# Performance work log

Hardware: AMD Instinct MI355X
Metric: run time of the kernel (lower is better)

The kernel has to match this reference:

```python
import jax, jax.numpy as jnp
import numpy as np

NH, NB, E, R, K, SU = 64, 384, 1024, 1024, 16, 64  # humans, boxes, enc size, repr size, cardinality, sub-repr
C, P, SPA = 256, 7, 36
NUM_ITER = 2


def _ln(x, g, b):
    m = jnp.mean(x, -1, keepdims=True)
    v = jnp.mean((x - m) ** 2, -1, keepdims=True)
    return (x - m) / jnp.sqrt(v + 1e-5) * g + b


def setup_inputs():
    key = jax.random.key(0)
    it = iter(jax.random.split(key, 48))
    def w(shape, scale=0.02):
        return jax.random.normal(next(it), shape, dtype=jnp.float32) * scale
    z = lambda *s: jnp.zeros(s, jnp.float32)
    return {
        "box_feats": jax.random.normal(next(it), (NB, C, P, P), dtype=jnp.float32),
        "spatial_raw": jax.random.uniform(next(it), (NH * NB, SPA), dtype=jnp.float32),
        "features3": jax.random.normal(next(it), (1, C, P, P), dtype=jnp.float32),
        "Wb1": w((C * P * P, E)), "bb1": z(E), "Wb2": w((E, E)), "bb2": z(E),
        "Ws1": w((SPA, 128)), "bs1": z(128), "Ws2": w((128, 256)), "bs2": z(256),
        "Ws3": w((256, 1024)), "bs3": z(1024),
        "Wadj": w((R, 1)), "badj": z(1),
        "gh": jnp.ones((E,), jnp.float32), "bh": z(E),
        "go": jnp.ones((E,), jnp.float32), "bo": z(E),
        "A1": w((K, 2 * E, SU)), "Ab1": z(K, SU), "A2": w((K, 1024, SU)), "Ab2": z(K, SU),
        "A3": w((K, SU, R)), "Ab3": z(K, R),
        "G1": w((K, 256, SU)), "Gb1": z(K, SU), "G2": w((K, 1024, SU)), "Gb2": z(K, SU),
        "G3": w((K, SU, R)), "Gb3": z(K, R),
        "S1": w((K, E, SU)), "Sb1": z(K, SU), "S2": w((K, 1024, SU)), "Sb2": z(K, SU),
        "S3": w((K, SU, R)), "Sb3": z(K, R),
        "O1": w((K, E, SU)), "Ob1": z(K, SU), "O2": w((K, 1024, SU)), "Ob2": z(K, SU),
        "O3": w((K, SU, R)), "Ob3": z(K, R),
        "n_h": NH,
    }


def _forward(box_feats, spatial_raw, features3, Wb1, bb1, Wb2, bb2, Ws1, bs1, Ws2, bs2, Ws3, bs3,
             Wadj, badj, gh, bh, go, bo, A1, Ab1, A2, Ab2, A3, Ab3, G1, Gb1, G2, Gb2, G3, Gb3,
             S1, Sb1, S2, Sb2, S3, Sb3, O1, Ob1, O2, Ob2, O3, Ob3, n_h):
    n = box_feats.shape[0]
    # box_head: Flatten -> Linear -> ReLU -> Linear -> ReLU
    enc = jax.nn.relu(jax.nn.relu(box_feats.reshape(n, -1) @ Wb1 + bb1) @ Wb2 + bb2)  # [n, E]
    h, o = enc[:n_h], enc
    # spatial_head MLP on flat pairs (pair p = i*n + j, human i, object j)
    sp = spatial_raw
    for W, b in ((Ws1, bs1), (Ws2, bs2), (Ws3, bs3)):
        sp = jax.nn.relu(sp @ W + b)                      # [n_h*n, 1024]
    spr = sp.reshape(n_h, n, -1)
    gfeat = features3.mean((2, 3))                        # AdaptiveAvgPool2d(1) -> [1, 256]

    def mbf(app, W1, b1, W2, b2, W3, b3):
        # MultiBranchFusion over flat pairs, K branches vectorized as batched GEMMs
        a = jnp.einsum('pa,kau->kpu', app, W1) + b1[:, None, :]
        s = jnp.einsum('ps,ksu->kpu', sp, W2) + b2[:, None, :]
        m = jax.nn.relu(a * s)                            # [K, P, sub]
        return jax.nn.relu(jnp.einsum('kpu,kur->pr', m, W3) + b3.sum(0))

    def pair_app(hh, oo):
        return jnp.concatenate([jnp.repeat(hh, n, axis=0), jnp.tile(oo, (n_h, 1))], axis=1)

    adj = jnp.ones((n_h, n), sp.dtype)
    for _ in range(NUM_ITER):
        wts = mbf(pair_app(h, o), A1, Ab1, A2, Ab2, A3, Ab3)      # [P, R]
        adj = (wts @ Wadj + badj).reshape(n_h, n)
        # MessageMBF object->subject (_forward_object_nodes): output [n_h, n, R], no final relu
        ao = jnp.einsum('na,kau->knu', o, O1) + Ob1[:, None, :]
        so = jnp.einsum('hns,ksu->khnu', spr, O2) + Ob2[:, None, None, :]
        m_o2s = jnp.einsum('khnu,kur->hnr', jax.nn.relu(ao[:, None] * so), O3) + Ob3.sum(0)
        h = _ln(h + jax.nn.relu(jnp.sum(jax.nn.softmax(adj, 1)[..., None] * m_o2s, axis=1)), gh, bh)
        # MessageMBF subject->object (_forward_human_nodes): output [n, n_h, R]
        ah = jnp.einsum('ha,kau->khu', h, S1) + Sb1[:, None, :]
        sh = jnp.einsum('hns,ksu->khnu', spr, S2) + Sb2[:, None, None, :]
        m_s2o = jnp.einsum('khnu,kur->nhr', jax.nn.relu(ah[:, :, None, :] * sh), S3) + Sb3.sum(0)
        o = _ln(o + jax.nn.relu(jnp.sum(jax.nn.softmax(adj.T, 1)[..., None] * m_s2o, axis=1)), go, bo)

    attn = mbf(pair_app(h, o), A1, Ab1, A2, Ab2, A3, Ab3)          # [P, R]
    gp = jnp.broadcast_to(gfeat, (sp.shape[0], gfeat.shape[1]))
    attn_g = mbf(gp, G1, Gb1, G2, Gb2, G3, Gb3)                    # [P, R]
    return jnp.concatenate([attn, attn_g], axis=1)                 # [P, 2R]


def reference(box_feats, spatial_raw, features3, Wb1, bb1, Wb2, bb2, Ws1, bs1, Ws2, bs2, Ws3, bs3,
              Wadj, badj, gh, bh, go, bo, A1, Ab1, A2, Ab2, A3, Ab3, G1, Gb1, G2, Gb2, G3, Gb3,
              S1, Sb1, S2, Sb2, S3, Sb3, O1, Ob1, O2, Ob2, O3, Ob3, n_h):
    return _forward(box_feats, spatial_raw, features3, Wb1, bb1, Wb2, bb2, Ws1, bs1, Ws2, bs2, Ws3, bs3,
                    Wadj, badj, gh, bh, go, bo, A1, Ab1, A2, Ab2, A3, Ab3, G1, Gb1, G2, Gb2, G3, Gb3,
                    S1, Sb1, S2, Sb2, S3, Sb3, O1, Ob1, O2, Ob2, O3, Ob3, n_h)
```

## Files before the change

### kernel.cpp

```cpp
#include <hip/hip_runtime.h>
#include <hip/hip_bf16.h>
#include <cstdint>
#include <cstddef>

#define NH    64
#define NB    384
#define EDIM  1024
#define PAIRS (NH*NB)
#define SPA   36

using in_t  = float;
using out_t = float;
using sb_t  = __hip_bfloat16;

typedef short bf16x8 __attribute__((ext_vector_type(8)));
typedef float f32x4  __attribute__((ext_vector_type(4)));

static __device__ __forceinline__ float cvt(float x){ return x; }
static __device__ __forceinline__ float cvt(__hip_bfloat16 x){ return __bfloat162float(x); }
static __device__ __forceinline__ void stv(float* p, float v){ *p = v; }
static __device__ __forceinline__ void stv(__hip_bfloat16* p, float v){ *p = __float2bfloat16(v); }

static __device__ __forceinline__ float b2f(unsigned short u){
  union { unsigned int i; float f; } x; x.i = ((unsigned int)u)<<16; return x.f;
}

typedef const __attribute__((address_space(1))) void* as1_t;
typedef __attribute__((address_space(3))) void* as3_t;
static __device__ __forceinline__ void gl_lds16(const void* g, void* l){
  __builtin_amdgcn_global_load_lds((as1_t)g, (as3_t)l, 16, 0, 0);
}

#define POOL_BB1   0
#define POOL_BB2   1024
#define POOL_BS1   2048
#define POOL_BS2   2176
#define POOL_BS3   2432
#define POOL_AB1   3456
#define POOL_GB1   4480
#define POOL_SB1   5504
#define POOL_OB1   6528
#define POOL_B2ALL 7552
#define POOL_AB3S  11648
#define POOL_GB3S  12672
#define POOL_SB3S  13696
#define POOL_OB3S  14720
#define POOL_GFEAT 15744
#define POOL_TOTAL 16000

template<int EPI, int RELU, typename TC>
__global__ __launch_bounds__(256)
void gemm_mfma(int M, int N, int KS, int lda, int ldb,
               const sb_t* __restrict__ A,
               const sb_t* __restrict__ Bt,
               const float* __restrict__ bias,
               TC* __restrict__ C, int ldc, int coff, long long strideCz,
               const float* __restrict__ Wadj,
               const float* __restrict__ ab3s,
               float* __restrict__ adjOut)
{
  __shared__ alignas(16) short lA[2][128*32];
  __shared__ alignas(16) short lB[2][128*32];
  const int tid = threadIdx.x;
  const int w = tid >> 6, l = tid & 63;
  const int m0 = blockIdx.x * 128, n0 = blockIdx.y * 128;
  const int wr = w >> 1, wc = w & 1;
  const int Koff = blockIdx.z * KS;

  const int srow = w*32 + (l>>2);
  const int scol = (l&3)*8;
  const sb_t* gA = A  + (size_t)(m0 + srow)*(size_t)lda + Koff + scol;
  const sb_t* gB = Bt + (size_t)(n0 + srow)*(size_t)ldb + Koff + scol;
  short* lA0 = &lA[0][(w*32)*32];
  short* lA1 = &lA[1][(w*32)*32];
  short* lB0 = &lB[0][(w*32)*32];
  short* lB1 = &lB[1][(w*32)*32];

  f32x4 acc[4][4];
  const f32x4 zz = {0.f,0.f,0.f,0.f};
  #pragma unroll
  for (int i=0;i<4;++i)
    #pragma unroll
    for (int j=0;j<4;++j) acc[i][j] = zz;

  const int fr  = l & 15;
  const int fko = (l >> 4) * 8;

  for (int k0 = 0; k0 < KS; k0 += 64) {
    gl_lds16(gA + k0,               lA0);
    gl_lds16(gA + k0 + 16*lda,      lA0 + 16*32);
    gl_lds16(gA + k0 + 32,          lA1);
    gl_lds16(gA + k0 + 32 + 16*lda, lA1 + 16*32);
    gl_lds16(gB + k0,               lB0);
    gl_lds16(gB + k0 + 16*ldb,      lB0 + 16*32);
    gl_lds16(gB + k0 + 32,          lB1);
    gl_lds16(gB + k0 + 32 + 16*ldb, lB1 + 16*32);
    __syncthreads();
    #pragma unroll
    for (int kh=0; kh<2; ++kh) {
      bf16x8 af[4], bfv[4];
      #pragma unroll
      for (int i=0;i<4;++i)
        af[i]  = *(const bf16x8*)&lA[kh][(wr*64 + i*16 + fr)*32 + fko];
      #pragma unroll
      for (int j=0;j<4;++j)
        bfv[j] = *(const bf16x8*)&lB[kh][(wc*64 + j*16 + fr)*32 + fko];
      #pragma unroll
      for (int i=0;i<4;++i)
        #pragma unroll
        for (int j=0;j<4;++j)
          acc[i][j] = __builtin_amdgcn_mfma_f32_16x16x32_bf16(af[i], bfv[j], acc[i][j], 0, 0, 0);
    }
    __syncthreads();
  }

  const int cn = l & 15;
  const int cr = (l >> 4) * 4;

  if (EPI == 1) {
    float part[4][4];
    #pragma unroll
    for (int i=0;i<4;++i)
      #pragma unroll
      for (int r=0;r<4;++r) part[i][r] = 0.f;
    #pragma unroll
    for (int j=0;j<4;++j) {
      const int col = n0 + wc*64 + j*16 + cn;
      const float wv = Wadj[col];
      const float bv = ab3s[col];
      #pragma unroll
      for (int i=0;i<4;++i)
        #pragma unroll
        for (int r=0;r<4;++r)
          part[i][r] += fmaxf(acc[i][j][r] + bv, 0.f) * wv;
    }
    #pragma unroll
    for (int m=1;m<16;m<<=1)
      #pragma unroll
      for (int i=0;i<4;++i)
        #pragma unroll
        for (int r=0;r<4;++r)
          part[i][r] += __shfl_xor(part[i][r], m, 64);
    if (cn == 0) {
      #pragma unroll
      for (int i=0;i<4;++i)
        #pragma unroll
        for (int r=0;r<4;++r)
          atomicAdd(&adjOut[m0 + wr*64 + i*16 + cr + r], part[i][r]);
    }
    return;
  }

  #pragma unroll
  for (int j=0;j<4;++j) {
    const int col = n0 + wc*64 + j*16 + cn;
    const float bv = (EPI==0 && bias) ? bias[col] : 0.f;
    #pragma unroll
    for (int i=0;i<4;++i) {
      #pragma unroll
      for (int r=0;r<4;++r) {
        const int row = m0 + wr*64 + i*16 + cr + r;
        float v = acc[i][j][r] + bv;
        if (RELU) v = fmaxf(v, 0.f);
        if (EPI == 2)
          stv(&C[(size_t)blockIdx.z*strideCz + (size_t)row*ldc + col], v);
        else
          stv(&C[(size_t)row*ldc + coff + col], v);
      }
    }
  }
}

template<int EPI, int RELU, typename TC>
__global__ __launch_bounds__(512, 2)
void gemm256(int M, int N, int K, int lda, int ldb,
             const sb_t* __restrict__ A,
             const sb_t* __restrict__ Bt,
             const float* __restrict__ bias,
             TC* __restrict__ C, int ldc, int coff,
             const float* __restrict__ Wadj,
             const float* __restrict__ ab3s,
             float* __restrict__ adjOut)
{
  __shared__ alignas(16) short sh[2][2][256*64];

  const int tid = threadIdx.x;
  const int w = tid >> 6, l = tid & 63;
  const int wr = w >> 2, wc = w & 3;

  const unsigned gx = gridDim.x, gy = gridDim.y;
  const unsigned nwg = gx * gy;
  const unsigned hwid = blockIdx.x + gx * blockIdx.y;
  const unsigned q = nwg >> 3, rr = nwg & 7;
  const unsigned xcd = hwid & 7, jj = hwid >> 3;
  const unsigned wg = (xcd < rr ? xcd*(q+1) : rr*(q+1) + (xcd-rr)*q) + jj;
  const int by = (int)(wg % gy), bx = (int)(wg / gy);
  const int m0 = bx * 256, n0 = by * 256;

  const int NT = K >> 6;

  const int lr = l >> 3;
  const int lch = ((l & 7) ^ lr) * 8;

  auto stage = [&](int p, int s, int t){
    short* lbA = &sh[p][0][0];
    short* lbB = &sh[p][1][0];
    const int k0 = t * 64;
    #pragma unroll
    for (int c=0;c<2;++c){
      const int g = (w<<1) + c;
      int row0; const sb_t* mat; int ld; int rb; short* dst;
      if (s==0){ row0 = g*8;                              mat=Bt; ld=ldb; rb=n0; dst=lbB; }
      else if (s==1){ row0 = 128 + g*8;                   mat=Bt; ld=ldb; rb=n0; dst=lbB; }
      else if (s==2){ row0 = (g<8)? g*8    : 128+(g-8)*8; mat=A;  ld=lda; rb=m0; dst=lbA; }
      else          { row0 = (g<8)? 64+g*8 : 192+(g-8)*8; mat=A;  ld=lda; rb=m0; dst=lbA; }
      gl_lds16(mat + (size_t)(rb + row0 + lr)*(size_t)ld + k0 + lch, dst + row0*64);
    }
  };

  const int fr = l & 15;
  const int fg = l >> 4;
  const int sx = fr & 7;
  const int x0 = ((0 + fg) ^ sx) * 8;
  const int x1 = ((4 + fg) ^ sx) * 8;
  const int oA = (wr*128 + fr) * 64;
  const int oB = (wc*64  + fr) * 64;

  f32x4 acc[8][4];
  const f32x4 zz = {0.f,0.f,0.f,0.f};
  #pragma unroll
  for (int i=0;i<8;++i)
    #pragma unroll
    for (int j=0;j<4;++j) acc[i][j] = zz;

#define G256_BAR()   __builtin_amdgcn_s_barrier()
#define G256_LGKM0() asm volatile("s_waitcnt lgkmcnt(0)" ::: "memory")
#define G256_LGKM8() asm volatile("s_waitcnt lgkmcnt(8)" ::: "memory")
#define G256_VM(n)   asm volatile("s_waitcnt vmcnt(" #n ")" ::: "memory")
#define G256_LOADA(ph)                                                   \
  af[0][0] = *(const bf16x8*)(sa + oA + (2*(ph)+0)*1024 + x0);           \
  af[0][1] = *(const bf16x8*)(sa + oA + (2*(ph)+0)*1024 + x1);           \
  af[1][0] = *(const bf16x8*)(sa + oA + (2*(ph)+1)*1024 + x0);           \
  af[1][1] = *(const bf16x8*)(sa + oA + (2*(ph)+1)*1024 + x1)
#define G256_MFMA(ph)                                                    \
  do { __builtin_amdgcn_s_setprio(1);                                    \
    _Pragma("unroll") for (int ii=0; ii<2; ++ii)                         \
    _Pragma("unroll") for (int j=0; j<4; ++j)                            \
    _Pragma("unroll") for (int kk=0; kk<2; ++kk)                         \
      acc[2*(ph)+ii][j] = __builtin_amdgcn_mfma_f32_16x16x32_bf16(       \
          af[ii][kk], bf[j][kk], acc[2*(ph)+ii][j], 0, 0, 0);            \
    __builtin_amdgcn_s_setprio(0); } while(0)

  stage(0,0,0); stage(0,1,0); stage(0,2,0); stage(0,3,0);
  G256_VM(4);
  if (NT > 1) {
    stage(1,0,1); stage(1,1,1); stage(1,2,1);
    G256_VM(6);
  } else {
    G256_VM(0);
  }
  G256_BAR();

  for (int t=0; t<NT; ++t) {
    const int cur = t & 1, pn = cur ^ 1;
    short* sa  = &sh[cur][0][0];
    short* sb2 = &sh[cur][1][0];
    bf16x8 bf[4][2], af[2][2];

    #pragma unroll
    for (int j=0;j<4;++j){
      bf[j][0] = *(const bf16x8*)(sb2 + oB + j*1024 + x0);
      bf[j][1] = *(const bf16x8*)(sb2 + oB + j*1024 + x1);
    }
    G256_LOADA(0);
    if (t+1 < NT) stage(pn, 3, t+1);
    G256_LGKM8();
    G256_BAR(); G256_LGKM0();
    G256_MFMA(0);
    G256_BAR();

    G256_LOADA(1);
    if (t+2 < NT) stage(cur, 0, t+2);
    G256_BAR(); G256_LGKM0();
    G256_MFMA(1);
    G256_BAR();

    G256_LOADA(2);
    if (t+2 < NT) stage(cur, 1, t+2);
    G256_BAR(); G256_LGKM0();
    G256_MFMA(2);
    G256_BAR();

    G256_LOADA(3);
    if (t+2 < NT) stage(cur, 2, t+2);
    G256_BAR(); G256_LGKM0();
    G256_MFMA(3);
    if (t+1 < NT) {
      if (t+2 < NT) { G256_VM(6); } else { G256_VM(0); }
      G256_BAR();
    }
  }

#undef G256_BAR
#undef G256_LGKM0
#undef G256_LGKM8
#undef G256_VM
#undef G256_LOADA
#undef G256_MFMA

  const int cn = l & 15;
  const int cr = (l >> 4) * 4;

  if (EPI == 1) {
    float part[8][4];
    #pragma unroll
    for (int i=0;i<8;++i)
      #pragma unroll
      for (int r=0;r<4;++r) part[i][r] = 0.f;
    #pragma unroll
    for (int j=0;j<4;++j) {
      const int col = n0 + wc*64 + j*16 + cn;
      const float wv = Wadj[col];
      const float bv = ab3s[col];
      #pragma unroll
      for (int i=0;i<8;++i)
        #pragma unroll
        for (int r=0;r<4;++r)
          part[i][r] += fmaxf(acc[i][j][r] + bv, 0.f) * wv;
    }
    #pragma unroll
    for (int m=1;m<16;m<<=1)
      #pragma unroll
      for (int i=0;i<8;++i)
        #pragma unroll
        for (int r=0;r<4;++r)
          part[i][r] += __shfl_xor(part[i][r], m, 64);
    if (cn == 0) {
      #pragma unroll
      for (int i=0;i<8;++i)
        #pragma unroll
        for (int r=0;r<4;++r)
          atomicAdd(&adjOut[m0 + wr*128 + i*16 + cr + r], part[i][r]);
    }
    return;
  }

  #pragma unroll
  for (int j=0;j<4;++j) {
    const int col = n0 + wc*64 + j*16 + cn;
    const float bv = bias ? bias[col] : 0.f;
    #pragma unroll
    for (int i=0;i<8;++i) {
      #pragma unroll
      for (int r=0;r<4;++r) {
        const int row = m0 + wr*128 + i*16 + cr + r;
        float v = acc[i][j][r] + bv;
        if (RELU) v = fmaxf(v, 0.f);
        stv(&C[(size_t)row*ldc + coff + col], v);
      }
    }
  }
}

template<typename TC>
__global__ __launch_bounds__(256)
void gemm_valu(int M, int N, int K,
               const in_t* __restrict__ S, int ldsS,
               const in_t* __restrict__ B, int ldb, long long strideB,
               const float* __restrict__ bias,
               TC* __restrict__ C, int ldc, int reluOut)
{
  __shared__ float As[16][65];
  __shared__ float Bs[16][68];
  const int z  = blockIdx.z;
  const in_t* Bz = B + (long long)z * strideB;
  const int m0 = blockIdx.x * 64;
  const int n0 = blockIdx.y * 64;
  const int tid = threadIdx.x;
  const int tx = tid & 15;
  const int ty = tid >> 4;

  float acc[4][4];
  #pragma unroll
  for (int i=0;i<4;++i)
    #pragma unroll
    for (int j=0;j<4;++j) acc[i][j]=0.f;

  const int kTiles = (K + 15) >> 4;
  for (int kt=0; kt<kTiles; ++kt) {
    const int k0 = kt << 4;
    #pragma unroll
    for (int q=0;q<4;++q) {
      const int p = m0 + ty + 16*q;
      const int c = k0 + tx;
      As[tx][ty+16*q] = (p < M && c < K) ? S[(size_t)p*ldsS + c] : 0.f;
    }
    {
      const int n = tid & 63;
      #pragma unroll
      for (int q=0;q<4;++q) {
        const int kk = (tid >> 6) + 4*q;
        const int gk = k0 + kk;
        const int gn = n0 + n;
        Bs[kk][n] = (gk < K && gn < N) ? Bz[(size_t)gk*ldb + gn] : 0.f;
      }
    }
    __syncthreads();
    #pragma unroll
    for (int kk=0; kk<16; ++kk) {
      float a[4], b[4];
      #pragma unroll
      for (int i=0;i<4;++i) a[i] = As[kk][ty + 16*i];
      #pragma unroll
      for (int j=0;j<4;++j) b[j] = Bs[kk][tx + 16*j];
      #pragma unroll
      for (int i=0;i<4;++i)
        #pragma unroll
        for (int j=0;j<4;++j) acc[i][j] += a[i]*b[j];
    }
    __syncthreads();
  }
  #pragma unroll
  for (int i=0;i<4;++i) {
    const int r = m0 + ty + 16*i;
    if (r >= M) continue;
    #pragma unroll
    for (int j=0;j<4;++j) {
      const int nn = n0 + tx + 16*j;
      if (nn >= N) continue;
      const int ccol = z*N + nn;
      float v = acc[i][j];
      if (bias) v += bias[ccol];
      if (reluOut) v = fmaxf(v, 0.f);
      stv(&C[(size_t)r*ldc + ccol], v);
    }
  }
}

struct Prep17 { const in_t* p[17]; };

__global__ __launch_bounds__(256)
void prep_kernel(Prep17 a, float* __restrict__ pool)
{
  const int len[17] = {1024,1024,128,256,1024,1024,1024,1024,1024,1024,1024,1024,1024,
                       1024,1024,1024,1024};
  const int off[17] = {POOL_BB1,POOL_BB2,POOL_BS1,POOL_BS2,POOL_BS3,POOL_AB1,
                       POOL_B2ALL+0,
                       POOL_GB1,
                       POOL_B2ALL+3072,
                       POOL_SB1,
                       POOL_B2ALL+2048,
                       POOL_OB1,
                       POOL_B2ALL+1024,
                       POOL_AB3S,POOL_GB3S,POOL_SB3S,POOL_OB3S};
  const int j = blockIdx.x;
  const in_t* src = a.p[j];
  const int L = len[j], o = off[j];
  for (int i = threadIdx.x; i < L; i += blockDim.x) {
    if (j < 13) {
      pool[o+i] = src[i];
    } else {
      float s = 0.f;
      for (int k=0;k<16;++k) s += src[k*1024 + i];
      pool[o+i] = s;
    }
  }
}

__global__ __launch_bounds__(64)
void gfeat_kernel(const in_t* __restrict__ f3, float* __restrict__ g)
{
  const int c = blockIdx.x;
  const int t = threadIdx.x;
  float s = (t < 49) ? f3[c*49 + t] : 0.f;
  #pragma unroll
  for (int o=32;o>0;o>>=1) s += __shfl_down(s, o, 64);
  if (t == 0) g[c] = s * (1.0f/49.0f);
}

__global__ __launch_bounds__(256)
void tcvt_kernel(const float* __restrict__ in, sb_t* __restrict__ outT, int R, int C)
{
  __shared__ float t[64][65];
  const int r0 = blockIdx.x*64, c0 = blockIdx.y*64;
  const int x = threadIdx.x & 63, y = threadIdx.x >> 6;
  #pragma unroll 4
  for (int q=0;q<16;++q){ const int rl = q*4 + y; t[rl][x] = in[(size_t)(r0+rl)*C + c0 + x]; }
  __syncthreads();
  #pragma unroll 4
  for (int q=0;q<16;++q){ const int cl = q*4 + y; stv(&outT[(size_t)(c0+cl)*R + r0 + x], t[x][cl]); }
}

__global__ __launch_bounds__(256)
void pack_kt_kernel(const float* __restrict__ W, sb_t* __restrict__ PT, int Cdim)
{
  __shared__ float t[64][65];
  const int c0 = blockIdx.x*64; const int k = blockIdx.y;
  const int x = threadIdx.x & 63, y = threadIdx.x >> 6;
  #pragma unroll 4
  for (int q=0;q<16;++q){ const int cl = q*4 + y; t[cl][x] = W[((size_t)k*Cdim + c0 + cl)*64 + x]; }
  __syncthreads();
  #pragma unroll 4
  for (int q=0;q<16;++q){ const int u = q*4 + y; stv(&PT[((size_t)k*64 + u)*Cdim + c0 + x], t[x][u]); }
}

__global__ void cvt_kernel(const float* __restrict__ in, sb_t* __restrict__ o, int n){
  const int i = blockIdx.x*256 + threadIdx.x;
  if (i < n) stv(&o[i], in[i]);
}

__global__ __launch_bounds__(256)
void combine4_kernel(const float* __restrict__ part, const float* __restrict__ bias,
                     sb_t* __restrict__ o)
{
  const int i = blockIdx.x*256 + threadIdx.x;
  const int c = i & 1023;
  float v = part[i] + part[i+393216] + part[i+2*393216] + part[i+3*393216] + bias[c];
  stv(&o[i], fmaxf(v, 0.f));
}

__global__ __launch_bounds__(256)
void encpost_kernel(const float* __restrict__ oB, sb_t* __restrict__ oBb,
                    float* __restrict__ hB, sb_t* __restrict__ hBb)
{
  const int p = blockIdx.x; const int c = blockIdx.y*256 + threadIdx.x;
  const float v = oB[(size_t)p*1024 + c];
  stv(&oBb[(size_t)p*1024+c], v);
  if (p < NH){ hB[(size_t)p*1024+c] = v; stv(&hBb[(size_t)p*1024+c], v); }
}

__global__ __launch_bounds__(256)
void mmake_kernel(const float* __restrict__ U, int hasU, int ldu,
                  const float* __restrict__ V, int hasV,
                  const sb_t* __restrict__ S, int ldS, int colOff,
                  sb_t* __restrict__ Mo)
{
  const int p = blockIdx.x;
  const int c = threadIdx.x * 4;
  const ushort4 sv = *(const ushort4*)((const unsigned short*)S + (size_t)p*ldS + colOff + c);
  float a0=0.f,a1=0.f,a2=0.f,a3=0.f;
  if (hasU){ const float* Up = U + (size_t)(p/NB)*ldu + c; a0=Up[0];a1=Up[1];a2=Up[2];a3=Up[3]; }
  if (hasV){ const float* Vp = V + (size_t)(p%NB)*1024 + c; a0+=Vp[0];a1+=Vp[1];a2+=Vp[2];a3+=Vp[3]; }
  __hip_bfloat16* mo = (__hip_bfloat16*)Mo + (size_t)p*1024 + c;
  mo[0] = __float2bfloat16(fmaxf(a0*b2f(sv.x),0.f));
  mo[1] = __float2bfloat16(fmaxf(a1*b2f(sv.y),0.f));
  mo[2] = __float2bfloat16(fmaxf(a2*b2f(sv.z),0.f));
  mo[3] = __float2bfloat16(fmaxf(a3*b2f(sv.w),0.f));
}

__global__ __launch_bounds__(512)
void smax_h_kernel(const float* __restrict__ adj, float* __restrict__ wh)
{
  __shared__ float red[512];
  const int hh = blockIdx.x, t = threadIdx.x;
  float av = (t < NB) ? adj[hh*NB + t] : -1e30f;
  red[t]=av; __syncthreads();
  for (int s=256;s>0;s>>=1){ if(t<s) red[t]=fmaxf(red[t],red[t+s]); __syncthreads(); }
  float mx = red[0]; __syncthreads();
  float e = (t < NB) ? __expf(av - mx) : 0.f;
  red[t]=e; __syncthreads();
  for (int s=256;s>0;s>>=1){ if(t<s) red[t]+=red[t+s]; __syncthreads(); }
  if (t < NB) wh[hh*NB + t] = e / red[0];
}

__global__ __launch_bounds__(64)
void smax_o_kernel(const float* __restrict__ adj, float* __restrict__ wo)
{
  const int n = blockIdx.x, t = threadIdx.x;
  float av = adj[t*NB + n];
  float mx = av;
  #pragma unroll
  for (int o=32;o>0;o>>=1) mx = fmaxf(mx, __shfl_xor(mx, o, 64));
  float e = __expf(av - mx);
  float s = e;
  #pragma unroll
  for (int o=32;o>0;o>>=1) s += __shfl_xor(s, o, 64);
  wo[n*64 + t] = e / s;
}

__global__ __launch_bounds__(128)
void wredH_kernel(const float* __restrict__ wh, const float* __restrict__ ao,
                  const sb_t* __restrict__ s4, int colOff, sb_t* __restrict__ mw)
{
  const int hh = blockIdx.x;
  const int c = blockIdx.y*128 + threadIdx.x;
  const unsigned short* sp = (const unsigned short*)s4 + (size_t)hh*NB*4096 + colOff + c;
  const float* whp = wh + hh*NB;
  float acc = 0.f;
  for (int n=0; n<NB; ++n)
    acc += whp[n] * fmaxf(ao[(size_t)n*1024 + c] * b2f(sp[(size_t)n*4096]), 0.f);
  stv(&mw[(size_t)hh*1024 + c], acc);
}

__global__ __launch_bounds__(128)
void wredO_kernel(const float* __restrict__ wo, const float* __restrict__ ah,
                  const sb_t* __restrict__ s4, int colOff, sb_t* __restrict__ mw)
{
  const int n = blockIdx.x;
  const int c = blockIdx.y*128 + threadIdx.x;
  const unsigned short* sp = (const unsigned short*)s4 + (size_t)n*4096 + colOff + c;
  const float* wop = wo + n*64;
  float acc = 0.f;
  for (int h=0; h<NH; ++h)
    acc += wop[h] * fmaxf(ah[(size_t)h*1024 + c] * b2f(sp[(size_t)h*NB*4096]), 0.f);
  stv(&mw[(size_t)n*1024 + c], acc);
}

static __device__ __forceinline__ float bsum(float v, float* red){
  const int t = threadIdx.x;
  red[t]=v; __syncthreads();
  for (int s=512;s>0;s>>=1){ if(t<s) red[t]+=red[t+s]; __syncthreads(); }
  float r = red[0]; __syncthreads();
  return r;
}

__global__ __launch_bounds__(1024)
void ln_update_kernel(const float* __restrict__ msg, const float* __restrict__ b3s,
                      const in_t* __restrict__ g, const in_t* __restrict__ b,
                      float* __restrict__ x, sb_t* __restrict__ xb)
{
  __shared__ float red[1024];
  const int row = blockIdx.x, t = threadIdx.x;
  float val = x[(size_t)row*1024 + t] + fmaxf(msg[(size_t)row*1024 + t] + b3s[t], 0.f);
  float mean = bsum(val, red) * (1.0f/1024.0f);
  float d = val - mean;
  float var = bsum(d*d, red) * (1.0f/1024.0f);
  float y = d * rsqrtf(var + 1e-5f) * g[t] + b[t];
  x[(size_t)row*1024 + t] = y;
  stv(&xb[(size_t)row*1024 + t], y);
}

template<int EPI, int RELU, typename TC>
static inline void launch_mfma(hipStream_t st, int M, int N, int KS, int lda, int ldb, int nz,
    const sb_t* A, const sb_t* Bt, const float* bias, TC* C, int ldc, int coff,
    long long strideCz, const float* Wadj, const float* ab3s, float* adjOut)
{
  dim3 g((unsigned)(M/128), (unsigned)(N/128), (unsigned)nz);
  hipLaunchKernelGGL((gemm_mfma<EPI,RELU,TC>), g, dim3(256), 0, st,
                     M,N,KS,lda,ldb,A,Bt,bias,C,ldc,coff,strideCz,Wadj,ab3s,adjOut);
}

template<int EPI, int RELU, typename TC>
static inline void launch_mfma256(hipStream_t st, int M, int N, int K, int lda, int ldb,
    const sb_t* A, const sb_t* Bt, const float* bias, TC* C, int ldc, int coff,
    const float* Wadj, const float* ab3s, float* adjOut)
{
  dim3 g((unsigned)(M/256), (unsigned)(N/256), 1);
  hipLaunchKernelGGL((gemm256<EPI,RELU,TC>), g, dim3(512), 0, st,
                     M,N,K,lda,ldb,A,Bt,bias,C,ldc,coff,Wadj,ab3s,adjOut);
}

extern "C" void kernel_launch(void* const* d_in, const int* in_sizes, int n_in,
                              void* d_out, int out_size, void* d_ws, size_t ws_size,
                              hipStream_t stream)
{
  (void)in_sizes; (void)n_in; (void)out_size; (void)ws_size;

  const in_t* box  = (const in_t*)d_in[0];
  const in_t* spat = (const in_t*)d_in[1];
  const in_t* f3   = (const in_t*)d_in[2];
  const in_t* Wb1  = (const in_t*)d_in[3];
  const in_t* Wb2  = (const in_t*)d_in[5];
  const in_t* Ws1  = (const in_t*)d_in[7];
  const in_t* Ws2  = (const in_t*)d_in[9];
  const in_t* Ws3  = (const in_t*)d_in[11];
  const in_t* Wadj = (const in_t*)d_in[13];
  const in_t* gh   = (const in_t*)d_in[15];
  const in_t* bh   = (const in_t*)d_in[16];
  const in_t* go   = (const in_t*)d_in[17];
  const in_t* bo   = (const in_t*)d_in[18];
  const in_t* A1   = (const in_t*)d_in[19];
  const in_t* A2   = (const in_t*)d_in[21];
  const in_t* A3   = (const in_t*)d_in[23];
  const in_t* G1   = (const in_t*)d_in[25];
  const in_t* G2   = (const in_t*)d_in[27];
  const in_t* G3   = (const in_t*)d_in[29];
  const in_t* S1   = (const in_t*)d_in[31];
  const in_t* S2   = (const in_t*)d_in[33];
  const in_t* S3   = (const in_t*)d_in[35];
  const in_t* O1   = (const in_t*)d_in[37];
  const in_t* O2   = (const in_t*)d_in[39];
  const in_t* O3   = (const in_t*)d_in[41];
  out_t* out = (out_t*)d_out;

  char* wsb = (char*)d_ws;
  size_t off = 0;
  auto alloc = [&](size_t bytes)->void* {
    void* p = wsb + off; off += (bytes + 255) & ~(size_t)255; return p;
  };
  float* pool   = (float*)alloc((size_t)POOL_TOTAL*4);
  sb_t* Wb1T    = (sb_t*)alloc((size_t)1024*12544*2);
  sb_t* Wb2T    = (sb_t*)alloc((size_t)1024*1024*2);
  sb_t* Ws2T    = (sb_t*)alloc((size_t)256*128*2);
  sb_t* Ws3T    = (sb_t*)alloc((size_t)1024*256*2);
  sb_t* A3T     = (sb_t*)alloc((size_t)1024*1024*2);
  sb_t* O3T     = (sb_t*)alloc((size_t)1024*1024*2);
  sb_t* S3T     = (sb_t*)alloc((size_t)1024*1024*2);
  sb_t* G3T     = (sb_t*)alloc((size_t)1024*1024*2);
  sb_t* s2Tall  = (sb_t*)alloc((size_t)4096*1024*2);
  sb_t* O1T     = (sb_t*)alloc((size_t)1024*1024*2);
  sb_t* S1T     = (sb_t*)alloc((size_t)1024*1024*2);
  sb_t* A1T     = (sb_t*)alloc((size_t)1024*2048*2);
  sb_t* boxb    = (sb_t*)alloc((size_t)NB*12544*2);
  float* encP   = (float*)alloc((size_t)4*NB*EDIM*4);
  sb_t* encMidb = (sb_t*)alloc((size_t)NB*EDIM*2);
  float* oB     = (float*)alloc((size_t)NB*EDIM*4);
  sb_t* oBb     = (sb_t*)alloc((size_t)NB*EDIM*2);
  float* hB     = (float*)alloc((size_t)NH*EDIM*4);
  sb_t* hBb     = (sb_t*)alloc((size_t)128*EDIM*2);
  sb_t* sp1b    = (sb_t*)alloc((size_t)PAIRS*128*2);
  sb_t* sp2b    = (sb_t*)alloc((size_t)PAIRS*256*2);
  sb_t* spFb    = (sb_t*)alloc((size_t)PAIRS*EDIM*2);
  sb_t* mbuf    = spFb;
  sb_t* s4      = (sb_t*)alloc((size_t)PAIRS*4096*2);
  float* ahA    = (float*)alloc((size_t)128*EDIM*4);
  float* aoA    = (float*)alloc((size_t)NB*EDIM*4);
  float* aoO    = (float*)alloc((size_t)NB*EDIM*4);
  float* ahS    = (float*)alloc((size_t)128*EDIM*4);
  float* aGv    = (float*)alloc((size_t)EDIM*4);
  float* adj    = (float*)alloc((size_t)PAIRS*4);
  float* wh     = (float*)alloc((size_t)PAIRS*4);
  float* wo     = (float*)alloc((size_t)PAIRS*4);
  sb_t* mwH     = (sb_t*)alloc((size_t)128*EDIM*2);
  sb_t* mwO     = (sb_t*)alloc((size_t)NB*EDIM*2);
  float* hmsg   = (float*)alloc((size_t)128*EDIM*4);
  float* omsg   = (float*)alloc((size_t)NB*EDIM*4);

  Prep17 pp;
  const int prepIdx[17] = {4,6,8,10,12,20,22,26,28,32,34,38,40,24,30,36,42};
  for (int i=0;i<17;++i) pp.p[i] = (const in_t*)d_in[prepIdx[i]];
  hipLaunchKernelGGL(prep_kernel, dim3(17), dim3(256), 0, stream, pp, pool);
  hipLaunchKernelGGL(gfeat_kernel, dim3(256), dim3(64), 0, stream, f3, pool + POOL_GFEAT);

  hipLaunchKernelGGL(tcvt_kernel, dim3(196,16), dim3(256), 0, stream, Wb1, Wb1T, 12544, 1024);
  hipLaunchKernelGGL(tcvt_kernel, dim3(16,16),  dim3(256), 0, stream, Wb2, Wb2T, 1024, 1024);
  hipLaunchKernelGGL(tcvt_kernel, dim3(2,4),    dim3(256), 0, stream, Ws2, Ws2T, 128, 256);
  hipLaunchKernelGGL(tcvt_kernel, dim3(4,16),   dim3(256), 0, stream, Ws3, Ws3T, 256, 1024);
  hipLaunchKernelGGL(tcvt_kernel, dim3(16,16),  dim3(256), 0, stream, A3, A3T, 1024, 1024);
  hipLaunchKernelGGL(tcvt_kernel, dim3(16,16),  dim3(256), 0, stream, O3, O3T, 1024, 1024);
  hipLaunchKernelGGL(tcvt_kernel, dim3(16,16),  dim3(256), 0, stream, S3, S3T, 1024, 1024);
  hipLaunchKernelGGL(tcvt_kernel, dim3(16,16),  dim3(256), 0, stream, G3, G3T, 1024, 1024);

  hipLaunchKernelGGL(pack_kt_kernel, dim3(16,16), dim3(256), 0, stream, A2, s2Tall,            1024);
  hipLaunchKernelGGL(pack_kt_kernel, dim3(16,16), dim3(256), 0, stream, O2, s2Tall+1024*1024,  1024);
  hipLaunchKernelGGL(pack_kt_kernel, dim3(16,16), dim3(256), 0, stream, S2, s2Tall+2048*1024,  1024);
  hipLaunchKernelGGL(pack_kt_kernel, dim3(16,16), dim3(256), 0, stream, G2, s2Tall+3072*1024,  1024);
  hipLaunchKernelGGL(pack_kt_kernel, dim3(16,16), dim3(256), 0, stream, O1, O1T, 1024);
  hipLaunchKernelGGL(pack_kt_kernel, dim3(16,16), dim3(256), 0, stream, S1, S1T, 1024);
  hipLaunchKernelGGL(pack_kt_kernel, dim3(32,16), dim3(256), 0, stream, A1, A1T, 2048);

  hipLaunchKernelGGL(cvt_kernel, dim3((NB*12544)/256), dim3(256), 0, stream, box, boxb, NB*12544);

  launch_mfma<2,0,float>(stream, NB, EDIM, 3136, 12544, 12544, 4,
      boxb, Wb1T, nullptr, encP, EDIM, 0, (long long)NB*EDIM, nullptr, nullptr, nullptr);
  hipLaunchKernelGGL(combine4_kernel, dim3(NB*EDIM/256), dim3(256), 0, stream,
                     encP, pool+POOL_BB1, encMidb);
  launch_mfma<0,1,float>(stream, NB, EDIM, EDIM, EDIM, EDIM, 1,
      encMidb, Wb2T, pool+POOL_BB2, oB, EDIM, 0, 0, nullptr, nullptr, nullptr);
  hipLaunchKernelGGL(encpost_kernel, dim3(NB,4), dim3(256), 0, stream, oB, oBb, hB, hBb);

  {
    dim3 g((PAIRS+63)/64, 2, 1);
    hipLaunchKernelGGL((gemm_valu<sb_t>), g, dim3(256), 0, stream,
        PAIRS, 128, SPA, spat, SPA, Ws1, 128, 0, pool+POOL_BS1, sp1b, 128, 1);
  }
  launch_mfma<0,1,sb_t>(stream, PAIRS, 256, 128, 128, 128, 1,
      sp1b, Ws2T, pool+POOL_BS2, sp2b, 256, 0, 0, nullptr, nullptr, nullptr);
  launch_mfma256<0,1,sb_t>(stream, PAIRS, EDIM, 256, 256, 256,
      sp2b, Ws3T, pool+POOL_BS3, spFb, EDIM, 0, nullptr, nullptr, nullptr);

  launch_mfma256<0,0,sb_t>(stream, PAIRS, 4096, EDIM, EDIM, EDIM,
      spFb, s2Tall, pool+POOL_B2ALL, s4, 4096, 0, nullptr, nullptr, nullptr);

  {
    dim3 g(1, 1, 16);
    hipLaunchKernelGGL((gemm_valu<float>), g, dim3(256), 0, stream,
        1, 64, 256, pool+POOL_GFEAT, 256, G1, 64, 16384, pool+POOL_GB1, aGv, EDIM, 0);
  }

  for (int it=0; it<2; ++it) {
    launch_mfma<0,0,float>(stream, 128, EDIM, EDIM, EDIM, 2048, 1,
        hBb, A1T, pool+POOL_AB1, ahA, EDIM, 0, 0, nullptr, nullptr, nullptr);
    launch_mfma<0,0,float>(stream, NB, EDIM, EDIM, EDIM, 2048, 1,
        oBb, A1T+1024, nullptr, aoA, EDIM, 0, 0, nullptr, nullptr, nullptr);
    hipLaunchKernelGGL(mmake_kernel, dim3(PAIRS), dim3(256), 0, stream,
                       ahA, 1, 1024, aoA, 1, s4, 4096, 0, mbuf);
    (void)hipMemsetAsync(adj, 0, (size_t)PAIRS*4, stream);
    launch_mfma256<1,0,float>(stream, PAIRS, EDIM, EDIM, EDIM, EDIM,
        mbuf, A3T, nullptr, (float*)nullptr, 0, 0, Wadj, pool+POOL_AB3S, adj);
    hipLaunchKernelGGL(smax_h_kernel, dim3(NH), dim3(512), 0, stream, adj, wh);
    hipLaunchKernelGGL(smax_o_kernel, dim3(NB), dim3(64), 0, stream, adj, wo);

    launch_mfma<0,0,float>(stream, NB, EDIM, EDIM, EDIM, EDIM, 1,
        oBb, O1T, pool+POOL_OB1, aoO, EDIM, 0, 0, nullptr, nullptr, nullptr);
    hipLaunchKernelGGL(wredH_kernel, dim3(NH,8), dim3(128), 0, stream,
                       wh, aoO, s4, 1024, mwH);
    launch_mfma<0,0,float>(stream, 128, EDIM, EDIM, EDIM, EDIM, 1,
        mwH, O3T, nullptr, hmsg, EDIM, 0, 0, nullptr, nullptr, nullptr);
    hipLaunchKernelGGL(ln_update_kernel, dim3(NH), dim3(1024), 0, stream,
                       hmsg, pool+POOL_OB3S, gh, bh, hB, hBb);

    launch_mfma<0,0,float>(stream, 128, EDIM, EDIM, EDIM, EDIM, 1,
        hBb, S1T, pool+POOL_SB1, ahS, EDIM, 0, 0, nullptr, nullptr, nullptr);
    hipLaunchKernelGGL(wredO_kernel, dim3(NB,8), dim3(128), 0, stream,
                       wo, ahS, s4, 2048, mwO);
    launch_mfma<0,0,float>(stream, NB, EDIM, EDIM, EDIM, EDIM, 1,
        mwO, S3T, nullptr, omsg, EDIM, 0, 0, nullptr, nullptr, nullptr);
    hipLaunchKernelGGL(ln_update_kernel, dim3(NB), dim3(1024), 0, stream,
                       omsg, pool+POOL_SB3S, go, bo, oB, oBb);
  }

  launch_mfma<0,0,float>(stream, 128, EDIM, EDIM, EDIM, 2048, 1,
      hBb, A1T, pool+POOL_AB1, ahA, EDIM, 0, 0, nullptr, nullptr, nullptr);
  launch_mfma<0,0,float>(stream, NB, EDIM, EDIM, EDIM, 2048, 1,
      oBb, A1T+1024, nullptr, aoA, EDIM, 0, 0, nullptr, nullptr, nullptr);
  hipLaunchKernelGGL(mmake_kernel, dim3(PAIRS), dim3(256), 0, stream,
                     ahA, 1, 1024, aoA, 1, s4, 4096, 0, mbuf);
  launch_mfma256<0,1,out_t>(stream, PAIRS, EDIM, EDIM, EDIM, EDIM,
      mbuf, A3T, pool+POOL_AB3S, out, 2048, 0, nullptr, nullptr, nullptr);

  hipLaunchKernelGGL(mmake_kernel, dim3(PAIRS), dim3(256), 0, stream,
                     aGv, 1, 0, nullptr, 0, s4, 4096, 3072, mbuf);
  launch_mfma256<0,1,out_t>(stream, PAIRS, EDIM, EDIM, EDIM, EDIM,
      mbuf, G3T, pool+POOL_GB3S, out, 2048, 1024, nullptr, nullptr, nullptr);
}
```

Before: 1.682 ms.

## Split-K skinny GEMMs, stage gemm256 epilogue through LDS, reorder MFMA loop

New measurement: 1.481 ms. -11.9%, faster.

```diff
diff --git a/kernel.cpp b/kernel.cpp
--- a/kernel.cpp
+++ b/kernel.cpp
@@ -244,9 +244,9 @@
   af[1][1] = *(const bf16x8*)(sa + oA + (2*(ph)+1)*1024 + x1)
 #define G256_MFMA(ph)                                                    \
   do { __builtin_amdgcn_s_setprio(1);                                    \
+    _Pragma("unroll") for (int kk=0; kk<2; ++kk)                         \
     _Pragma("unroll") for (int ii=0; ii<2; ++ii)                         \
     _Pragma("unroll") for (int j=0; j<4; ++j)                            \
-    _Pragma("unroll") for (int kk=0; kk<2; ++kk)                         \
       acc[2*(ph)+ii][j] = __builtin_amdgcn_mfma_f32_16x16x32_bf16(       \
           af[ii][kk], bf[j][kk], acc[2*(ph)+ii][j], 0, 0, 0);            \
     __builtin_amdgcn_s_setprio(0); } while(0)
@@ -301,65 +301,112 @@
     }
   }
 
+#undef G256_LOADA
+#undef G256_MFMA
+
+  const int cn = l & 15;
+  const int cr = (l >> 4) * 4;
+
+  if (EPI == 1) {
+    float part[8][4];
+    #pragma unroll
+    for (int i=0;i<8;++i)
+      #pragma unroll
+      for (int r=0;r<4;++r) part[i][r] = 0.f;
+    #pragma unroll
+    for (int j=0;j<4;++j) {
+      const int col = n0 + wc*64 + j*16 + cn;
+      const float wv = Wadj[col];
+      const float bv = ab3s[col];
+      #pragma unroll
+      for (int i=0;i<8;++i)
+        #pragma unroll
+        for (int r=0;r<4;++r)
+          part[i][r] += fmaxf(acc[i][j][r] + bv, 0.f) * wv;
+    }
+    #pragma unroll
+    for (int m=1;m<16;m<<=1)
+      #pragma unroll
+      for (int i=0;i<8;++i)
+        #pragma unroll
+        for (int r=0;r<4;++r)
+          part[i][r] += __shfl_xor(part[i][r], m, 64);
+    if (cn == 0) {
+      #pragma unroll
+      for (int i=0;i<8;++i)
+        #pragma unroll
+        for (int r=0;r<4;++r)
+          atomicAdd(&adjOut[m0 + wr*128 + i*16 + cr + r], part[i][r]);
+    }
+    return;
+  }
+
+  if constexpr (sizeof(TC) == 2) {
+    sb_t* ebs = (sb_t*)&sh[0][0][0];
+    G256_LGKM0();
+    G256_BAR();
+    #pragma unroll
+    for (int i=0;i<8;++i){
+      const int lrow = wr*128 + i*16 + cr;
+      #pragma unroll
+      for (int j=0;j<4;++j){
+        const int lcol = wc*64 + j*16 + cn;
+        const float bv = bias ? bias[n0 + lcol] : 0.f;
+        #pragma unroll
+        for (int r=0;r<4;++r){
+          float v = acc[i][j][r] + bv;
+          if (RELU) v = fmaxf(v, 0.f);
+          stv(&ebs[(lrow+r)*256 + lcol], v);
+        }
+      }
+    }
+    G256_LGKM0();
+    G256_BAR();
+    #pragma unroll
+    for (int p=0;p<16;++p){
+      const int lrow = p*16 + (tid>>5);
+      const int sc = (tid&31)*8;
+      bf16x8 v = *(const bf16x8*)((const short*)ebs + lrow*256 + sc);
+      *(bf16x8*)((short*)C + (size_t)(m0+lrow)*ldc + coff + n0 + sc) = v;
+    }
+  } else {
+    float* ebf = (float*)&sh[0][0][0];
+    #pragma unroll
+    for (int h=0; h<2; ++h){
+      G256_LGKM0();
+      G256_BAR();
+      if (wr == h){
+        #pragma unroll
+        for (int i=0;i<8;++i){
+          const int lrow = i*16 + cr;
+          #pragma unroll
+          for (int j=0;j<4;++j){
+            const int lcol = wc*64 + j*16 + cn;
+            const float bv = bias ? bias[n0 + lcol] : 0.f;
+            #pragma unroll
+            for (int r=0;r<4;++r){
+              float v = acc[i][j][r] + bv;
+              if (RELU) v = fmaxf(v, 0.f);
+              ebf[(lrow+r)*256 + lcol] = v;
+            }
+          }
+        }
+      }
+      G256_LGKM0();
+      G256_BAR();
+      #pragma unroll
+      for (int p=0;p<16;++p){
+        const int lrow = p*8 + (tid>>6);
+        const int sc = (tid&63)*4;
+        f32x4 v = *(const f32x4*)&ebf[lrow*256 + sc];
+        *(f32x4*)((float*)C + (size_t)(m0 + h*128 + lrow)*ldc + coff + n0 + sc) = v;
+      }
+    }
+  }
 #undef G256_BAR
 #undef G256_LGKM0
 #undef G256_LGKM8
 #undef G256_VM
-#undef G256_LOADA
-#undef G256_MFMA
-
-  const int cn = l & 15;
-  const int cr = (l >> 4) * 4;
-
-  if (EPI == 1) {
-    float part[8][4];
-    #pragma unroll
-    for (int i=0;i<8;++i)
-      #pragma unroll
-      for (int r=0;r<4;++r) part[i][r] = 0.f;
-    #pragma unroll
-    for (int j=0;j<4;++j) {
-      const int col = n0 + wc*64 + j*16 + cn;
-      const float wv = Wadj[col];
-      const float bv = ab3s[col];
-      #pragma unroll
-      for (int i=0;i<8;++i)
-        #pragma unroll
-        for (int r=0;r<4;++r)
-          part[i][r] += fmaxf(acc[i][j][r] + bv, 0.f) * wv;
-    }
-    #pragma unroll
-    for (int m=1;m<16;m<<=1)
-      #pragma unroll
-      for (int i=0;i<8;++i)
-        #pragma unroll
-        for (int r=0;r<4;++r)
-          part[i][r] += __shfl_xor(part[i][r], m, 64);
-    if (cn == 0) {
-      #pragma unroll
-      for (int i=0;i<8;++i)
-        #pragma unroll
-        for (int r=0;r<4;++r)
-          atomicAdd(&adjOut[m0 + wr*128 + i*16 + cr + r], part[i][r]);
-    }
-    return;
-  }
-
-  #pragma unroll
-  for (int j=0;j<4;++j) {
-    const int col = n0 + wc*64 + j*16 + cn;
-    const float bv = bias ? bias[col] : 0.f;
-    #pragma unroll
-    for (int i=0;i<8;++i) {
-      #pragma unroll
-      for (int r=0;r<4;++r) {
-        const int row = m0 + wr*128 + i*16 + cr + r;
-        float v = acc[i][j][r] + bv;
-        if (RELU) v = fmaxf(v, 0.f);
-        stv(&C[(size_t)row*ldc + coff + col], v);
-      }
-    }
-  }
 }
 
 template<typename TC>
@@ -520,6 +567,18 @@
 }
 
 __global__ __launch_bounds__(256)
+void combineN_kernel(const float* __restrict__ part, long long stride, int nz,
+                     const float* __restrict__ bias, int N, int relu,
+                     float* __restrict__ out)
+{
+  const int i = blockIdx.x*256 + threadIdx.x;
+  float v = bias ? bias[i & (N-1)] : 0.f;
+  for (int z=0; z<nz; ++z) v += part[(long long)z*stride + i];
+  if (relu) v = fmaxf(v, 0.f);
+  out[i] = v;
+}
+
+__global__ __launch_bounds__(256)
 void encpost_kernel(const float* __restrict__ oB, sb_t* __restrict__ oBb,
                     float* __restrict__ hB, sb_t* __restrict__ hBb)
 {
@@ -648,6 +707,15 @@
   dim3 g((unsigned)(M/256), (unsigned)(N/256), 1);
   hipLaunchKernelGGL((gemm256<EPI,RELU,TC>), g, dim3(512), 0, st,
                      M,N,K,lda,ldb,A,Bt,bias,C,ldc,coff,Wadj,ab3s,adjOut);
+}
+
+static inline void launch_skinny(hipStream_t st, int M, int N, int K, int lda, int ldb, int nz,
+    const sb_t* A, const sb_t* Bt, const float* bias, float* outp, int relu, float* scratch)
+{
+  launch_mfma<2,0,float>(st, M, N, K/nz, lda, ldb, nz, A, Bt, nullptr, scratch, N, 0,
+                         (long long)M*N, nullptr, nullptr, nullptr);
+  hipLaunchKernelGGL(combineN_kernel, dim3((unsigned)((M*N)/256)), dim3(256), 0, st,
+                     scratch, (long long)M*N, nz, bias, N, relu, outp);
 }
 
 extern "C" void kernel_launch(void* const* d_in, const int* in_sizes, int n_in,
@@ -755,8 +823,8 @@
       boxb, Wb1T, nullptr, encP, EDIM, 0, (long long)NB*EDIM, nullptr, nullptr, nullptr);
   hipLaunchKernelGGL(combine4_kernel, dim3(NB*EDIM/256), dim3(256), 0, stream,
                      encP, pool+POOL_BB1, encMidb);
-  launch_mfma<0,1,float>(stream, NB, EDIM, EDIM, EDIM, EDIM, 1,
-      encMidb, Wb2T, pool+POOL_BB2, oB, EDIM, 0, 0, nullptr, nullptr, nullptr);
+  launch_skinny(stream, NB, EDIM, EDIM, EDIM, EDIM, 4,
+      encMidb, Wb2T, pool+POOL_BB2, oB, 1, encP);
   hipLaunchKernelGGL(encpost_kernel, dim3(NB,4), dim3(256), 0, stream, oB, oBb, hB, hBb);
 
   {
@@ -779,10 +847,10 @@
   }
 
   for (int it=0; it<2; ++it) {
-    launch_mfma<0,0,float>(stream, 128, EDIM, EDIM, EDIM, 2048, 1,
-        hBb, A1T, pool+POOL_AB1, ahA, EDIM, 0, 0, nullptr, nullptr, nullptr);
-    launch_mfma<0,0,float>(stream, NB, EDIM, EDIM, EDIM, 2048, 1,
-        oBb, A1T+1024, nullptr, aoA, EDIM, 0, 0, nullptr, nullptr, nullptr);
+    launch_skinny(stream, 128, EDIM, EDIM, EDIM, 2048, 8,
+        hBb, A1T, pool+POOL_AB1, ahA, 0, encP);
+    launch_skinny(stream, NB, EDIM, EDIM, EDIM, 2048, 4,
+        oBb, A1T+1024, nullptr, aoA, 0, encP);
     hipLaunchKernelGGL(mmake_kernel, dim3(PAIRS), dim3(256), 0, stream,
                        ahA, 1, 1024, aoA, 1, s4, 4096, 0, mbuf);
     (void)hipMemsetAsync(adj, 0, (size_t)PAIRS*4, stream);
@@ -791,29 +859,29 @@
     hipLaunchKernelGGL(smax_h_kernel, dim3(NH), dim3(512), 0, stream, adj, wh);
     hipLaunchKernelGGL(smax_o_kernel, dim3(NB), dim3(64), 0, stream, adj, wo);
 
-    launch_mfma<0,0,float>(stream, NB, EDIM, EDIM, EDIM, EDIM, 1,
-        oBb, O1T, pool+POOL_OB1, aoO, EDIM, 0, 0, nullptr, nullptr, nullptr);
+    launch_skinny(stream, NB, EDIM, EDIM, EDIM, 1024, 4,
+        oBb, O1T, pool+POOL_OB1, aoO, 0, encP);
     hipLaunchKernelGGL(wredH_kernel, dim3(NH,8), dim3(128), 0, stream,
                        wh, aoO, s4, 1024, mwH);
-    launch_mfma<0,0,float>(stream, 128, EDIM, EDIM, EDIM, EDIM, 1,
-        mwH, O3T, nullptr, hmsg, EDIM, 0, 0, nullptr, nullptr, nullptr);
+    launch_skinny(stream, 128, EDIM, EDIM, EDIM, 1024, 8,
+        mwH, O3T, nullptr, hmsg, 0, encP);
     hipLaunchKernelGGL(ln_update_kernel, dim3(NH), dim3(1024), 0, stream,
                        hmsg, pool+POOL_OB3S, gh, bh, hB, hBb);
 
-    launch_mfma<0,0,float>(stream, 128, EDIM, EDIM, EDIM, EDIM, 1,
-        hBb, S1T, pool+POOL_SB1, ahS, EDIM, 0, 0, nullptr, nullptr, nullptr);
+    launch_skinny(stream, 128, EDIM, EDIM, EDIM, 1024, 8,
+        hBb, S1T, pool+POOL_SB1, ahS, 0, encP);
     hipLaunchKernelGGL(wredO_kernel, dim3(NB,8), dim3(128), 0, stream,
                        wo, ahS, s4, 2048, mwO);
-    launch_mfma<0,0,float>(stream, NB, EDIM, EDIM, EDIM, EDIM, 1,
-        mwO, S3T, nullptr, omsg, EDIM, 0, 0, nullptr, nullptr, nullptr);
+    launch_skinny(stream, NB, EDIM, EDIM, EDIM, 1024, 4,
+        mwO, S3T, nullptr, omsg, 0, encP);
     hipLaunchKernelGGL(ln_update_kernel, dim3(NB), dim3(1024), 0, stream,
                        omsg, pool+POOL_SB3S, go, bo, oB, oBb);
   }
 
-  launch_mfma<0,0,float>(stream, 128, EDIM, EDIM, EDIM, 2048, 1,
-      hBb, A1T, pool+POOL_AB1, ahA, EDIM, 0, 0, nullptr, nullptr, nullptr);
-  launch_mfma<0,0,float>(stream, NB, EDIM, EDIM, EDIM, 2048, 1,
-      oBb, A1T+1024, nullptr, aoA, EDIM, 0, 0, nullptr, nullptr, nullptr);
+  launch_skinny(stream, 128, EDIM, EDIM, EDIM, 2048, 8,
+      hBb, A1T, pool+POOL_AB1, ahA, 0, encP);
+  launch_skinny(stream, NB, EDIM, EDIM, EDIM, 2048, 4,
+      oBb, A1T+1024, nullptr, aoA, 0, encP);
   hipLaunchKernelGGL(mmake_kernel, dim3(PAIRS), dim3(256), 0, stream,
                      ahA, 1, 1024, aoA, 1, s4, 4096, 0, mbuf);
   launch_mfma256<0,1,out_t>(stream, PAIRS, EDIM, EDIM, EDIM, EDIM,
```
